# Performance work log

Hardware: AMD Instinct MI355X
Metric: run time of the kernel (lower is better)

The kernel has to match this reference:

```python
import jax, jax.numpy as jnp
import numpy as np

COMMITMENT_COST = 0.25


def setup_inputs() -> dict:
    key = jax.random.key(0)
    k1, k2 = jax.random.split(key)
    B, H, W, D, K = 64, 32, 32, 64, 1024
    x = jax.random.normal(k1, (B, H, W, D), dtype=jnp.float32)
    # variance_scaling(fan_in=D, uniform) ~ U(-sqrt(3/D), sqrt(3/D)); plain normal*scale is fine for a reference
    embeddings = jax.random.uniform(k2, (D, K), dtype=jnp.float32,
                                    minval=-np.sqrt(3.0 / D), maxval=np.sqrt(3.0 / D))
    return {"x": x, "embeddings": embeddings}


def reference(x, embeddings):
    D = embeddings.shape[0]
    K = embeddings.shape[1]
    flat = x.reshape(-1, D)                                   # [N, D]
    # squared euclidean distance: ||f||^2 - 2 f.E + ||e||^2 -> [N, K]
    distance = (jnp.sum(flat ** 2, axis=1, keepdims=True)
                - 2.0 * jnp.matmul(flat, embeddings)
                + jnp.sum(embeddings ** 2, axis=0, keepdims=True))
    encoding_indices_flat = jnp.argmax(-distance, axis=1)     # [N]
    encodings = jax.nn.one_hot(encoding_indices_flat, K, dtype=distance.dtype)  # [N, K]
    encoding_indices = encoding_indices_flat.reshape(x.shape[:-1])
    # quantize: gather rows of E^T -> same shape as x
    quantized = jnp.take(embeddings.T, encoding_indices, axis=0)
    e_latent_loss = jnp.mean((jax.lax.stop_gradient(quantized) - x) ** 2)
    q_latent_loss = jnp.mean((quantized - jax.lax.stop_gradient(x)) ** 2)
    loss = q_latent_loss + COMMITMENT_COST * e_latent_loss
    quantized_st = x + jax.lax.stop_gradient(quantized - x)   # straight-through
    avg_probs = jnp.mean(encodings, axis=0)                   # [K]
    perplexity = jnp.exp(-jnp.sum(avg_probs * jnp.log(avg_probs + 1e-10)))
    return quantized_st, loss, perplexity, encoding_indices
```

## Files before the change

kernel.cpp:

```cpp
#include <hip/hip_runtime.h>
#include <math.h>


typedef __attribute__((ext_vector_type(8))) short short8v;
typedef __attribute__((ext_vector_type(4))) float float4v;
typedef unsigned short u16;
typedef unsigned int u32;

constexpr int D = 64;
constexpr int K = 1024;
constexpr int NPTS = 65536;
constexpr long QOFF = (long)NPTS * D;
constexpr float BIAS = 24.0f;
constexpr float GATE = 5e-3f;

constexpr size_t OFF_LOSS = 0;
constexpr size_t OFF_CNT  = 256;
constexpr size_t OFF_EC   = OFF_CNT + 4096;
constexpr size_t OFF_ECB  = OFF_EC + 4096;
constexpr size_t OFF_ET   = OFF_ECB + 4096;
constexpr size_t OFF_H2   = OFF_ET + (size_t)K * D * 4;
constexpr size_t OFF_L2   = OFF_H2 + (size_t)K * D * 2;
constexpr size_t WS_ZERO  = OFF_CNT + 4096;

__device__ __forceinline__ float med3(float a, float b, float c) {
  return __builtin_amdgcn_fmed3f(a, b, c);
}
__device__ __forceinline__ u16 bf16rtn(float x) {
  u32 u = __float_as_uint(x);
  return (u16)((u + 0x7fffu + ((u >> 16) & 1u)) >> 16);
}
__device__ __forceinline__ float bf2f(u16 h) {
  return __uint_as_float(((u32)h) << 16);
}

__global__ __launch_bounds__(256) void prep_norm(const float* __restrict__ E,
                                                 float* __restrict__ eC,
                                                 float* __restrict__ eCb) {
  int k = blockIdx.x * 256 + threadIdx.x;
  float c = __fmul_rn(E[k], E[k]);
#pragma unroll
  for (int d = 1; d < D; ++d) {
    float v = E[d * K + k];
    c = __fadd_rn(c, __fmul_rn(v, v));
  }
  eC[k] = c;
  eCb[k] = c + BIAS;
}

__global__ __launch_bounds__(256) void prep_conv(const float* __restrict__ E,
                                                 float* __restrict__ Et,
                                                 u16* __restrict__ h2,
                                                 u16* __restrict__ l2) {
  int gid = blockIdx.x * 256 + threadIdx.x;
  int k = gid & 1023;
  int dg = gid >> 10;
#pragma unroll
  for (int i = 0; i < 4; ++i) {
    int d = dg * 4 + i;
    float v = E[d * K + k];
    Et[(size_t)k * 64 + d] = v;
    float m2 = -2.0f * v;
    u16 h = bf16rtn(m2);
    u16 l = bf16rtn(m2 - bf2f(h));
    h2[(size_t)k * 64 + d] = h;
    l2[(size_t)k * 64 + d] = l;
  }
}

__global__ __launch_bounds__(256) void vq_main(const float* __restrict__ x,
                                               const float* __restrict__ E,
                                               const u16* __restrict__ h2g,
                                               const u16* __restrict__ l2g,
                                               const float* __restrict__ eC,
                                               const float* __restrict__ eCb,
                                               const float* __restrict__ Etg,
                                               float* __restrict__ out,
                                               double* __restrict__ lossSum,
                                               int* __restrict__ counts) {
  __shared__ __align__(16) u16 hA[128 * 72];
  __shared__ __align__(16) u16 lA[128 * 72];
  __shared__ __align__(16) float ecb[128];
  __shared__ __align__(16) float topbuf[256 * 4];
  __shared__ int bkbuf[128];

  const int tid = threadIdx.x;
  const int w = tid >> 6;
  const int lane = tid & 63;
  const int col = lane & 15;
  const int quad = lane >> 4;
  const int blockBase = blockIdx.x * 128;
  const float INF = __builtin_inff();

  short8v Bh[2][2], Bl[2][2];
#pragma unroll
  for (int pt = 0; pt < 2; ++pt) {
    const float* xp = x + (size_t)(blockBase + w * 32 + pt * 16 + col) * 64;
#pragma unroll
    for (int s = 0; s < 2; ++s) {
      const float4* src = (const float4*)(xp + s * 32 + quad * 8);
      float4 a = src[0], b = src[1];
      float xs[8] = {a.x, a.y, a.z, a.w, b.x, b.y, b.z, b.w};
      short8v hf, lf;
#pragma unroll
      for (int j = 0; j < 8; ++j) {
        u16 h = bf16rtn(xs[j]);
        hf[j] = (short)h;
        lf[j] = (short)bf16rtn(xs[j] - bf2f(h));
      }
      Bh[pt][s] = hf;
      Bl[pt][s] = lf;
    }
  }

  float b1[2] = {INF, INF}, b2[2] = {INF, INF};

  for (int ch = 0; ch < 8; ++ch) {
    const int kbase = ch * 128;
    __syncthreads();
#pragma unroll
    for (int i = 0; i < 4; ++i) {
      int idx = tid + i * 256;
      int k = idx >> 3, dg = idx & 7;
      *(float4*)&hA[k * 72 + dg * 8] =
          *(const float4*)&h2g[(size_t)(kbase + k) * 64 + dg * 8];
      *(float4*)&lA[k * 72 + dg * 8] =
          *(const float4*)&l2g[(size_t)(kbase + k) * 64 + dg * 8];
    }
    if (tid < 32) *(float4*)&ecb[tid * 4] = *(const float4*)&eCb[kbase + tid * 4];
    __syncthreads();

#pragma unroll
    for (int ct = 0; ct < 8; ++ct) {
      const int rowbase = (ct * 16 + col) * 72;
      short8v Ah0 = *(const short8v*)&hA[rowbase + quad * 8];
      short8v Ah1 = *(const short8v*)&hA[rowbase + 32 + quad * 8];
      short8v Al0 = *(const short8v*)&lA[rowbase + quad * 8];
      short8v Al1 = *(const short8v*)&lA[rowbase + 32 + quad * 8];
      float4v Ci = *(const float4v*)&ecb[ct * 16 + quad * 4];
#pragma unroll
      for (int pt = 0; pt < 2; ++pt) {
        float4v C = Ci;
        C = __builtin_amdgcn_mfma_f32_16x16x32_bf16(Ah0, Bh[pt][0], C, 0, 0, 0);
        C = __builtin_amdgcn_mfma_f32_16x16x32_bf16(Ah1, Bh[pt][1], C, 0, 0, 0);
        C = __builtin_amdgcn_mfma_f32_16x16x32_bf16(Al0, Bh[pt][0], C, 0, 0, 0);
        C = __builtin_amdgcn_mfma_f32_16x16x32_bf16(Al1, Bh[pt][1], C, 0, 0, 0);
        C = __builtin_amdgcn_mfma_f32_16x16x32_bf16(Ah0, Bl[pt][0], C, 0, 0, 0);
        C = __builtin_amdgcn_mfma_f32_16x16x32_bf16(Ah1, Bl[pt][1], C, 0, 0, 0);
#pragma unroll
        for (int r = 0; r < 4; ++r) {
          u32 u = (__float_as_uint(C[r]) & 0xffffff00u) |
                  (u32)(ch * 32 + ct * 4 + r);
          float v = __uint_as_float(u);
          float pb = b1[pt];
          b1[pt] = fminf(pb, v);
          b2[pt] = med3(pb, b2[pt], v);
        }
      }
    }
  }

  topbuf[tid * 4 + 0] = b1[0];
  topbuf[tid * 4 + 1] = b2[0];
  topbuf[tid * 4 + 2] = b1[1];
  topbuf[tid * 4 + 3] = b2[1];
  __syncthreads();

  if (tid < 128) {
    const int mw = tid >> 5, mpt = (tid >> 4) & 1, mcol = tid & 15;
    float cv[8];
    int cq[8];
    float mv0 = INF, mv1 = INF;
    int q0 = 0;
#pragma unroll
    for (int q = 0; q < 4; ++q) {
      int lbase = (mw * 64 + q * 16 + mcol) * 4 + mpt * 2;
#pragma unroll
      for (int j = 0; j < 2; ++j) {
        float v = topbuf[lbase + j];
        cv[q * 2 + j] = v;
        cq[q * 2 + j] = q;
        if (v < mv0) { mv1 = mv0; mv0 = v; q0 = q; }
        else if (v < mv1) { mv1 = v; }
      }
    }
    u32 lb = __float_as_uint(mv0) & 255u;
    int bestk = (int)((lb >> 5) * 128 + ((lb >> 2) & 7) * 16 + q0 * 4 + (lb & 3));

    if (mv1 - mv0 < GATE) {
      const float* f = x + (size_t)(blockBase + tid) * 64;
      float r8[8];
#pragma unroll
      for (int j = 0; j < 8; ++j) { float fv = f[j]; r8[j] = __fmul_rn(fv, fv); }
#pragma unroll
      for (int i = 8; i < D; i += 8)
#pragma unroll
        for (int j = 0; j < 8; ++j) {
          float fv = f[i + j];
          r8[j] = __fadd_rn(r8[j], __fmul_rn(fv, fv));
        }
      float A = __fadd_rn(__fadd_rn(__fadd_rn(r8[0], r8[1]), __fadd_rn(r8[2], r8[3])),
                          __fadd_rn(__fadd_rn(r8[4], r8[5]), __fadd_rn(r8[6], r8[7])));
      float bd = INF;
      int bkk = K;
#pragma unroll
      for (int c = 0; c < 8; ++c) {
        u32 cb = __float_as_uint(cv[c]) & 255u;
        int k = (int)((cb >> 5) * 128 + ((cb >> 2) & 7) * 16 + cq[c] * 4 + (cb & 3));
        float m = 0.f;
#pragma unroll
        for (int d = 0; d < D; ++d) m = __fmaf_rn(f[d], E[d * K + k], m);
        float dist = __fadd_rn(__fsub_rn(A, __fmul_rn(2.f, m)), eC[k]);
        bool better = (dist < bd) || (dist == bd && k < bkk);
        bd = better ? dist : bd;
        bkk = better ? k : bkk;
      }
      bestk = bkk;
    }

    bkbuf[tid] = bestk;
    out[QOFF + 2 + blockBase + tid] = (float)bestk;
    atomicAdd(&counts[bestk], 1);
  }
  __syncthreads();

  const int pp = tid >> 1, half = tid & 1;
  const int bk = bkbuf[pp];
  const float4* et = (const float4*)(Etg + (size_t)bk * 64 + half * 32);
  const float4* xr = (const float4*)(x + (size_t)(blockBase + pp) * 64 + half * 32);
  float4* ov = (float4*)(out + (size_t)(blockBase + pp) * 64 + half * 32);
  float errs = 0.f;
#pragma unroll
  for (int i = 0; i < 8; ++i) {
    float4 qv = et[i];
    float4 xv = xr[i];
    float dx;
    dx = qv.x - xv.x; errs = fmaf(dx, dx, errs);
    dx = qv.y - xv.y; errs = fmaf(dx, dx, errs);
    dx = qv.z - xv.z; errs = fmaf(dx, dx, errs);
    dx = qv.w - xv.w; errs = fmaf(dx, dx, errs);
    ov[i] = qv;
  }
  double de = (double)errs;
#pragma unroll
  for (int off = 32; off > 0; off >>= 1) de += __shfl_down(de, off, 64);
  if (lane == 0) atomicAdd(lossSum, de);
}

__global__ __launch_bounds__(256) void vq_finalize(const double* __restrict__ lossSum,
                                                   const int* __restrict__ counts,
                                                   float* __restrict__ out) {
  __shared__ double sh[256];
  double ent = 0.0;
  for (int k = threadIdx.x; k < K; k += 256) {
    double pp = (double)counts[k] / (double)NPTS;
    ent += pp * log(pp + 1e-10);
  }
  sh[threadIdx.x] = ent;
  __syncthreads();
  for (int s = 128; s > 0; s >>= 1) {
    if (threadIdx.x < s) sh[threadIdx.x] += sh[threadIdx.x + s];
    __syncthreads();
  }
  if (threadIdx.x == 0) {
    out[QOFF + 0] = (float)(1.25 * (*lossSum) / (double)((long)NPTS * D));
    out[QOFF + 1] = (float)exp(-sh[0]);
  }
}

extern "C" void kernel_launch(void* const* d_in, const int* in_sizes, int n_in,
                              void* d_out, int out_size, void* d_ws, size_t ws_size,
                              hipStream_t stream) {
  const float* x = (const float*)d_in[0];
  const float* E = (const float*)d_in[1];
  float* out = (float*)d_out;

  char* ws = (char*)d_ws;
  double* lossSum = (double*)(ws + OFF_LOSS);
  int* counts = (int*)(ws + OFF_CNT);
  float* eC = (float*)(ws + OFF_EC);
  float* eCb = (float*)(ws + OFF_ECB);
  float* Etg = (float*)(ws + OFF_ET);
  u16* h2g = (u16*)(ws + OFF_H2);
  u16* l2g = (u16*)(ws + OFF_L2);

  hipMemsetAsync(d_ws, 0, WS_ZERO, stream);

  prep_norm<<<K / 256, 256, 0, stream>>>(E, eC, eCb);
  prep_conv<<<(K * 16) / 256, 256, 0, stream>>>(E, Etg, h2g, l2g);
  vq_main<<<NPTS / 128, 256, 0, stream>>>(x, E, h2g, l2g, eC, eCb, Etg, out,
                                          lossSum, counts);
  vq_finalize<<<1, 256, 0, stream>>>(lossSum, counts, out);
}
```

Measured before the change: 135.4 us.

## Double-buffer codebook via async global-to-LDS loads and merge prep kernels

Fuses the two prep kernels and the memset into one prep kernel. That kernel writes the bf16 hi/lo codebook in a pre-swizzled, chunk-contiguous staging layout and zeroes the counters itself. The main kernel now streams 32KB codebook chunks into double-buffered LDS with global_load_lds, prefetching two chunks ahead under manual waitcnt/barrier control, and keeps all 1024 biased norms in LDS. It also splits the MFMA accumulation into two independent chains to shorten dependency latency, and rescoring reads the transposed codebook rows. The aim is to remove per-chunk synchronous staging, launch overhead and bank conflicts, at the cost of about 72KB of LDS, which lowers occupancy, and fragile hand-written synchronisation.

```diff
diff --git a/kernel.cpp b/kernel.cpp
--- a/kernel.cpp
+++ b/kernel.cpp
@@ -19,9 +19,7 @@
 constexpr size_t OFF_EC   = OFF_CNT + 4096;
 constexpr size_t OFF_ECB  = OFF_EC + 4096;
 constexpr size_t OFF_ET   = OFF_ECB + 4096;
-constexpr size_t OFF_H2   = OFF_ET + (size_t)K * D * 4;
-constexpr size_t OFF_L2   = OFF_H2 + (size_t)K * D * 2;
-constexpr size_t WS_ZERO  = OFF_CNT + 4096;
+constexpr size_t OFF_STG  = OFF_ET + (size_t)K * D * 4;
 
 __device__ __forceinline__ float med3(float a, float b, float c) {
   return __builtin_amdgcn_fmed3f(a, b, c);
@@ -33,54 +31,69 @@
 __device__ __forceinline__ float bf2f(u16 h) {
   return __uint_as_float(((u32)h) << 16);
 }
-
-__global__ __launch_bounds__(256) void prep_norm(const float* __restrict__ E,
-                                                 float* __restrict__ eC,
-                                                 float* __restrict__ eCb) {
-  int k = blockIdx.x * 256 + threadIdx.x;
-  float c = __fmul_rn(E[k], E[k]);
-#pragma unroll
-  for (int d = 1; d < D; ++d) {
-    float v = E[d * K + k];
-    c = __fadd_rn(c, __fmul_rn(v, v));
-  }
-  eC[k] = c;
-  eCb[k] = c + BIAS;
-}
-
-__global__ __launch_bounds__(256) void prep_conv(const float* __restrict__ E,
-                                                 float* __restrict__ Et,
-                                                 u16* __restrict__ h2,
-                                                 u16* __restrict__ l2) {
+__device__ __forceinline__ void gl_lds16(const void* g, void* l) {
+  __builtin_amdgcn_global_load_lds(
+      (const __attribute__((address_space(1))) u32*)g,
+      (__attribute__((address_space(3))) u32*)l, 16, 0, 0);
+}
+
+__global__ __launch_bounds__(256) void vq_prep(const float* __restrict__ E,
+                                               float* __restrict__ eC,
+                                               float* __restrict__ eCb,
+                                               float* __restrict__ Et,
+                                               unsigned char* __restrict__ stg,
+                                               double* __restrict__ lossSum,
+                                               int* __restrict__ counts) {
   int gid = blockIdx.x * 256 + threadIdx.x;
+  int s = gid >> 10;
   int k = gid & 1023;
-  int dg = gid >> 10;
-#pragma unroll
-  for (int i = 0; i < 4; ++i) {
-    int d = dg * 4 + i;
-    float v = E[d * K + k];
-    Et[(size_t)k * 64 + d] = v;
-    float m2 = -2.0f * v;
-    u16 h = bf16rtn(m2);
-    u16 l = bf16rtn(m2 - bf2f(h));
-    h2[(size_t)k * 64 + d] = h;
-    l2[(size_t)k * 64 + d] = l;
+  size_t rowb = (size_t)(k >> 7) * 32768 + (size_t)(k & 127) * 256;
+  int swz = (k & 7) * 16;
+#pragma unroll
+  for (int q = 0; q < 4; ++q) {
+    float v[8];
+#pragma unroll
+    for (int j = 0; j < 8; ++j) v[j] = E[(s * 32 + q * 8 + j) * K + k];
+    *(float4*)&Et[(size_t)k * 64 + s * 32 + q * 8] =
+        make_float4(v[0], v[1], v[2], v[3]);
+    *(float4*)&Et[(size_t)k * 64 + s * 32 + q * 8 + 4] =
+        make_float4(v[4], v[5], v[6], v[7]);
+    short8v hv, lv;
+#pragma unroll
+    for (int j = 0; j < 8; ++j) {
+      float m2 = -2.0f * v[j];
+      u16 h = bf16rtn(m2);
+      hv[j] = (short)h;
+      lv[j] = (short)bf16rtn(m2 - bf2f(h));
+    }
+    int off = (s * 64 + q * 16) ^ swz;
+    *(short8v*)&stg[rowb + off] = hv;
+    *(short8v*)&stg[rowb + 128 + off] = lv;
+  }
+  if (s == 0) {
+    float c = __fmul_rn(E[k], E[k]);
+#pragma unroll
+    for (int d = 1; d < D; ++d) {
+      float vv = E[d * K + k];
+      c = __fadd_rn(c, __fmul_rn(vv, vv));
+    }
+    eC[k] = c;
+    eCb[k] = c + BIAS;
+    counts[k] = 0;
+    if (k == 0) *lossSum = 0.0;
   }
 }
 
 __global__ __launch_bounds__(256) void vq_main(const float* __restrict__ x,
-                                               const float* __restrict__ E,
-                                               const u16* __restrict__ h2g,
-                                               const u16* __restrict__ l2g,
+                                               const unsigned char* __restrict__ stg,
                                                const float* __restrict__ eC,
                                                const float* __restrict__ eCb,
                                                const float* __restrict__ Etg,
                                                float* __restrict__ out,
                                                double* __restrict__ lossSum,
                                                int* __restrict__ counts) {
-  __shared__ __align__(16) u16 hA[128 * 72];
-  __shared__ __align__(16) u16 lA[128 * 72];
-  __shared__ __align__(16) float ecb[128];
+  __shared__ __align__(16) unsigned char sbuf[2][32768];
+  __shared__ __align__(16) float ecb[1024];
   __shared__ __align__(16) float topbuf[256 * 4];
   __shared__ int bkbuf[128];
 
@@ -92,6 +105,8 @@
   const int blockBase = blockIdx.x * 128;
   const float INF = __builtin_inff();
 
+  *(float4*)&ecb[tid * 4] = *(const float4*)&eCb[tid * 4];
+
   short8v Bh[2][2], Bl[2][2];
 #pragma unroll
   for (int pt = 0; pt < 2; ++pt) {
@@ -113,43 +128,48 @@
     }
   }
 
+  {
+    const unsigned char* s0 = stg + (size_t)tid * 16;
+#pragma unroll
+    for (int i = 0; i < 8; ++i)
+      gl_lds16(s0 + i * 4096, &sbuf[0][tid * 16 + i * 4096]);
+#pragma unroll
+    for (int i = 0; i < 8; ++i)
+      gl_lds16(s0 + 32768 + i * 4096, &sbuf[1][tid * 16 + i * 4096]);
+  }
+  asm volatile("s_waitcnt vmcnt(8) lgkmcnt(0)" ::: "memory");
+  __builtin_amdgcn_s_barrier();
+  __builtin_amdgcn_sched_barrier(0);
+  asm volatile("" ::: "memory");
+
   float b1[2] = {INF, INF}, b2[2] = {INF, INF};
-
+  const int swz = (col & 7) * 16;
+
+#pragma unroll 1
   for (int ch = 0; ch < 8; ++ch) {
-    const int kbase = ch * 128;
-    __syncthreads();
-#pragma unroll
-    for (int i = 0; i < 4; ++i) {
-      int idx = tid + i * 256;
-      int k = idx >> 3, dg = idx & 7;
-      *(float4*)&hA[k * 72 + dg * 8] =
-          *(const float4*)&h2g[(size_t)(kbase + k) * 64 + dg * 8];
-      *(float4*)&lA[k * 72 + dg * 8] =
-          *(const float4*)&l2g[(size_t)(kbase + k) * 64 + dg * 8];
-    }
-    if (tid < 32) *(float4*)&ecb[tid * 4] = *(const float4*)&eCb[kbase + tid * 4];
-    __syncthreads();
-
+    unsigned char* bufB = sbuf[ch & 1];
 #pragma unroll
     for (int ct = 0; ct < 8; ++ct) {
-      const int rowbase = (ct * 16 + col) * 72;
-      short8v Ah0 = *(const short8v*)&hA[rowbase + quad * 8];
-      short8v Ah1 = *(const short8v*)&hA[rowbase + 32 + quad * 8];
-      short8v Al0 = *(const short8v*)&lA[rowbase + quad * 8];
-      short8v Al1 = *(const short8v*)&lA[rowbase + 32 + quad * 8];
-      float4v Ci = *(const float4v*)&ecb[ct * 16 + quad * 4];
+      const int rb = ct * 4096 + col * 256;
+      short8v Ah0 = *(const short8v*)&bufB[rb + ((quad * 16) ^ swz)];
+      short8v Ah1 = *(const short8v*)&bufB[rb + ((64 + quad * 16) ^ swz)];
+      short8v Al0 = *(const short8v*)&bufB[rb + 128 + ((quad * 16) ^ swz)];
+      short8v Al1 = *(const short8v*)&bufB[rb + 128 + ((64 + quad * 16) ^ swz)];
+      float4v Ci = *(const float4v*)&ecb[ch * 128 + ct * 16 + quad * 4];
 #pragma unroll
       for (int pt = 0; pt < 2; ++pt) {
-        float4v C = Ci;
-        C = __builtin_amdgcn_mfma_f32_16x16x32_bf16(Ah0, Bh[pt][0], C, 0, 0, 0);
-        C = __builtin_amdgcn_mfma_f32_16x16x32_bf16(Ah1, Bh[pt][1], C, 0, 0, 0);
-        C = __builtin_amdgcn_mfma_f32_16x16x32_bf16(Al0, Bh[pt][0], C, 0, 0, 0);
-        C = __builtin_amdgcn_mfma_f32_16x16x32_bf16(Al1, Bh[pt][1], C, 0, 0, 0);
-        C = __builtin_amdgcn_mfma_f32_16x16x32_bf16(Ah0, Bl[pt][0], C, 0, 0, 0);
-        C = __builtin_amdgcn_mfma_f32_16x16x32_bf16(Ah1, Bl[pt][1], C, 0, 0, 0);
+        float4v Ca = Ci;
+        float4v Cb = {0.f, 0.f, 0.f, 0.f};
+        Ca = __builtin_amdgcn_mfma_f32_16x16x32_bf16(Ah0, Bh[pt][0], Ca, 0, 0, 0);
+        Cb = __builtin_amdgcn_mfma_f32_16x16x32_bf16(Ah1, Bh[pt][1], Cb, 0, 0, 0);
+        Ca = __builtin_amdgcn_mfma_f32_16x16x32_bf16(Al0, Bh[pt][0], Ca, 0, 0, 0);
+        Cb = __builtin_amdgcn_mfma_f32_16x16x32_bf16(Al1, Bh[pt][1], Cb, 0, 0, 0);
+        Ca = __builtin_amdgcn_mfma_f32_16x16x32_bf16(Ah0, Bl[pt][0], Ca, 0, 0, 0);
+        Cb = __builtin_amdgcn_mfma_f32_16x16x32_bf16(Ah1, Bl[pt][1], Cb, 0, 0, 0);
 #pragma unroll
         for (int r = 0; r < 4; ++r) {
-          u32 u = (__float_as_uint(C[r]) & 0xffffff00u) |
+          float dv = Ca[r] + Cb[r];
+          u32 u = (__float_as_uint(dv) & 0xffffff00u) |
                   (u32)(ch * 32 + ct * 4 + r);
           float v = __uint_as_float(u);
           float pb = b1[pt];
@@ -157,6 +177,24 @@
           b2[pt] = med3(pb, b2[pt], v);
         }
       }
+    }
+    asm volatile("s_waitcnt lgkmcnt(0)" ::: "memory");
+    __builtin_amdgcn_s_barrier();
+    __builtin_amdgcn_sched_barrier(0);
+    asm volatile("" ::: "memory");
+    if (ch < 6) {
+      const unsigned char* s2 = stg + (size_t)(ch + 2) * 32768 + (size_t)tid * 16;
+#pragma unroll
+      for (int i = 0; i < 8; ++i)
+        gl_lds16(s2 + i * 4096, &bufB[tid * 16 + i * 4096]);
+      asm volatile("s_waitcnt vmcnt(8)" ::: "memory");
+    } else if (ch == 6) {
+      asm volatile("s_waitcnt vmcnt(0)" ::: "memory");
+    }
+    if (ch < 7) {
+      __builtin_amdgcn_s_barrier();
+      __builtin_amdgcn_sched_barrier(0);
+      asm volatile("" ::: "memory");
     }
   }
 
@@ -207,9 +245,10 @@
       for (int c = 0; c < 8; ++c) {
         u32 cb = __float_as_uint(cv[c]) & 255u;
         int k = (int)((cb >> 5) * 128 + ((cb >> 2) & 7) * 16 + cq[c] * 4 + (cb & 3));
+        const float* er = Etg + (size_t)k * 64;
         float m = 0.f;
 #pragma unroll
-        for (int d = 0; d < D; ++d) m = __fmaf_rn(f[d], E[d * K + k], m);
+        for (int d = 0; d < D; ++d) m = __fmaf_rn(f[d], er[d], m);
         float dist = __fadd_rn(__fsub_rn(A, __fmul_rn(2.f, m)), eC[k]);
         bool better = (dist < bd) || (dist == bd && k < bkk);
         bd = better ? dist : bd;
@@ -281,14 +320,10 @@
   float* eC = (float*)(ws + OFF_EC);
   float* eCb = (float*)(ws + OFF_ECB);
   float* Etg = (float*)(ws + OFF_ET);
-  u16* h2g = (u16*)(ws + OFF_H2);
-  u16* l2g = (u16*)(ws + OFF_L2);
-
-  hipMemsetAsync(d_ws, 0, WS_ZERO, stream);
-
-  prep_norm<<<K / 256, 256, 0, stream>>>(E, eC, eCb);
-  prep_conv<<<(K * 16) / 256, 256, 0, stream>>>(E, Etg, h2g, l2g);
-  vq_main<<<NPTS / 128, 256, 0, stream>>>(x, E, h2g, l2g, eC, eCb, Etg, out,
+  unsigned char* stgb = (unsigned char*)(ws + OFF_STG);
+
+  vq_prep<<<8, 256, 0, stream>>>(E, eC, eCb, Etg, stgb, lossSum, counts);
+  vq_main<<<NPTS / 128, 256, 0, stream>>>(x, stgb, eC, eCb, Etg, out,
                                           lossSum, counts);
   vq_finalize<<<1, 256, 0, stream>>>(lossSum, counts, out);
 }
```

Measured after the change: 142.2 us. 5.0% more time.
